# Kernel tuning notes

Hardware: AMD Instinct MI355X
Metric: run time of the kernel (lower is better)

The kernel has to match this reference:

```python
import jax, jax.numpy as jnp
from jax import lax
import numpy as np

B, F_BINS, T_TOTAL = 32, 128, 2400
H = 256           # cell_size
SEG = 24          # segment_size
S = T_TOTAL // SEG  # num_segments (T divisible by SEG)
SCALE = 1.0 / np.sqrt(H)


def _lstm_params(key, in_dim, hid_dim):
    k1, k2, k3, k4 = jax.random.split(key, 4)
    return (jax.random.normal(k1, (4 * hid_dim, in_dim), jnp.float32) * SCALE,
            jax.random.normal(k2, (4 * hid_dim, hid_dim), jnp.float32) * SCALE,
            jax.random.normal(k3, (4 * hid_dim,), jnp.float32) * SCALE,
            jax.random.normal(k4, (4 * hid_dim,), jnp.float32) * SCALE)


def setup_inputs() -> dict:
    key = jax.random.key(0)
    ks = jax.random.split(key, 5)
    inp = jax.random.normal(ks[0], (B, F_BINS, T_TOTAL), jnp.float32)
    oe = _lstm_params(ks[1], F_BINS, H)   # outer_encoder
    ie = _lstm_params(ks[2], H, H)        # inner_encoder
    idp = _lstm_params(ks[3], H, H)       # inner_decoder
    od = _lstm_params(ks[4], H, F_BINS)   # outer_decoder (hidden = input_size)
    d = {"inp": inp}
    for name, p in (("oe", oe), ("ie", ie), ("id", idp), ("od", od)):
        d[f"{name}_wih"], d[f"{name}_whh"], d[f"{name}_bih"], d[f"{name}_bhh"] = p
    return d


def run_lstm(x, w_ih, w_hh, b_ih, b_hh):
    """torch nn.LSTM (1 layer, batch_first). x: (N, T, I) -> outputs (N,T,Hd), h_T, c_T."""
    N = x.shape[0]
    Hd = w_hh.shape[1]
    # precompute input contribution for all steps: (N, T, 4H)
    xw = jnp.einsum('nti,gi->ntg', x, w_ih) + b_ih + b_hh

    def step(carry, xg):
        h, c = carry
        g = xg + h @ w_hh.T              # (N, 4H), gate order i,f,g,o
        i, f, gg, o = jnp.split(g, 4, axis=-1)
        c = jax.nn.sigmoid(f) * c + jax.nn.sigmoid(i) * jnp.tanh(gg)
        h = jax.nn.sigmoid(o) * jnp.tanh(c)
        return (h, c), h

    h0 = jnp.zeros((N, Hd), x.dtype)
    (hT, cT), ys = lax.scan(step, (h0, h0), jnp.swapaxes(xw, 0, 1))
    return jnp.swapaxes(ys, 0, 1), hT, cT


def reference(inp, oe_wih, oe_whh, oe_bih, oe_bhh,
              ie_wih, ie_whh, ie_bih, ie_bhh,
              id_wih, id_whh, id_bih, id_bhh,
              od_wih, od_whh, od_bih, od_bhh):
    x = jnp.swapaxes(inp, 1, 2)                      # (B, T, F)
    # outer encoder: all segments batched (independent in the original loop)
    segs = x.reshape(B * S, SEG, F_BINS)
    _, _, c_seg = run_lstm(segs, oe_wih, oe_whh, oe_bih, oe_bhh)   # (B*S, H)
    cell_state_tensor = c_seg.reshape(B, S, H)
    # inner encoder over segment cell-states -> bottleneck cell
    _, _, bottleneck = run_lstm(cell_state_tensor, ie_wih, ie_whh, ie_bih, ie_bhh)  # (B, H)
    # inner decoder: bottleneck repeated num_segments times
    dec_in = jnp.broadcast_to(bottleneck[:, None, :], (B, S, H))
    dec_out, _, _ = run_lstm(dec_in, id_wih, id_whh, id_bih, id_bhh)  # (B, S, H)
    # outer decoder: each segment code repeated SEG steps, batched over segments
    od_in = jnp.broadcast_to(dec_out.reshape(B * S, 1, H), (B * S, SEG, H))
    rec, _, _ = run_lstm(od_in, od_wih, od_whh, od_bih, od_bhh)       # (B*S, SEG, F)
    rec = rec.reshape(B, T_TOTAL, F_BINS)
    return jnp.swapaxes(rec, 1, 2)                   # (B, F, T)
```

## Files before the change

kernel.cpp:

```cpp
#include <hip/hip_runtime.h>


#define B_    32
#define F_    128
#define T_    2400
#define H_    256
#define SEG_  24
#define S_    100
#define NSEQ_ 3200

using v2h = __attribute__((ext_vector_type(2))) _Float16;
using v4h = __attribute__((ext_vector_type(4))) _Float16;
using v8h = __attribute__((ext_vector_type(8))) _Float16;
using v4f = __attribute__((ext_vector_type(4))) float;

#ifndef __has_builtin
#define __has_builtin(x) 0
#endif

__device__ __forceinline__ float fdot2f(v2h a, v2h b, float c) {
#if __has_builtin(__builtin_amdgcn_fdot2)
  return __builtin_amdgcn_fdot2(a, b, c, false);
#else
  return c + (float)a[0] * (float)b[0] + (float)a[1] * (float)b[1];
#endif
}

__device__ __forceinline__ v2h ext8(v8h v, int e) {
  v2h r; r[0] = v[2 * e]; r[1] = v[2 * e + 1]; return r;
}
__device__ __forceinline__ v2h ext4(v4h v, int e) {
  v2h r; r[0] = v[2 * e]; r[1] = v[2 * e + 1]; return r;
}

__device__ __forceinline__ float sigm(float x) { return 1.f / (1.f + __expf(-x)); }
__device__ __forceinline__ float tanh_f(float x) { return 1.f - 2.f / (__expf(2.f * x) + 1.f); }

__global__ void k_wt2(v2h* __restrict__ dst, const float* __restrict__ w1, int K1,
                      const float* __restrict__ w2, int K2src, int G, int n) {
  int idx = blockIdx.x * 256 + threadIdx.x;
  if (idx >= n) return;
  int k2 = idx / G, g = idx - k2 * G;
  int k = 2 * k2;
  float v0, v1;
  if (k < K1) {
    v0 = w1[(size_t)g * K1 + k];
    v1 = w1[(size_t)g * K1 + k + 1];
  } else {
    int kk = k - K1;
    v0 = w2[(size_t)g * K2src + kk];
    v1 = w2[(size_t)g * K2src + kk + 1];
  }
  v2h r;
  r[0] = (_Float16)v0;
  r[1] = (_Float16)v1;
  dst[idx] = r;
}

__global__ void k_f16(_Float16* __restrict__ dst, const float* __restrict__ src, int n) {
  int i = blockIdx.x * 256 + threadIdx.x;
  if (i < n) dst[i] = (_Float16)src[i];
}

__global__ void k_wpack_oe(v8h* __restrict__ dst, const float* __restrict__ wih,
                           const float* __restrict__ whh) {
  int idx = blockIdx.x * 256 + threadIdx.x;
  if (idx >= 12 * 64 * 64) return;
  int lane = idx & 63;
  int nt = (idx >> 6) & 63;
  int kc = idx >> 12;
  int col = nt * 16 + (lane & 15);
  int k0 = kc * 32 + (lane >> 4) * 8;
  v8h r;
#pragma unroll
  for (int j = 0; j < 8; ++j) {
    int k = k0 + j;
    float v = (k < 128) ? wih[(size_t)col * 128 + k] : whh[(size_t)col * 256 + (k - 128)];
    r[j] = (_Float16)v;
  }
  dst[idx] = r;
}

__global__ void k_wpack_od(v8h* __restrict__ dst, const float* __restrict__ whh) {
  int idx = blockIdx.x * 256 + threadIdx.x;
  if (idx >= 4 * 32 * 64) return;
  int lane = idx & 63;
  int nt = (idx >> 6) & 31;
  int kc = idx >> 11;
  int col = nt * 16 + (lane & 15);
  int k0 = kc * 32 + (lane >> 4) * 8;
  v8h r;
#pragma unroll
  for (int j = 0; j < 8; ++j) r[j] = (_Float16)whh[(size_t)col * 128 + k0 + j];
  dst[idx] = r;
}

__global__ void k_tin(const float* __restrict__ inp, _Float16* __restrict__ xT) {
  __shared__ float tile[32][33];
  int b = blockIdx.z, f0 = blockIdx.y * 32, t0 = blockIdx.x * 32;
  int tx = threadIdx.x, ty = threadIdx.y;
#pragma unroll
  for (int r = 0; r < 4; ++r) {
    int f = f0 + ty + 8 * r;
    tile[ty + 8 * r][tx] = inp[((size_t)b * F_ + f) * T_ + t0 + tx];
  }
  __syncthreads();
#pragma unroll
  for (int r = 0; r < 4; ++r) {
    int tau = t0 + ty + 8 * r;
    xT[((size_t)b * T_ + tau) * F_ + f0 + tx] = (_Float16)tile[tx][ty + 8 * r];
  }
}

__global__ void k_tout(const float* __restrict__ rec, float* __restrict__ out) {
  __shared__ float tile[32][33];
  int b = blockIdx.z, f0 = blockIdx.y * 32, t0 = blockIdx.x * 32;
  int tx = threadIdx.x, ty = threadIdx.y;
#pragma unroll
  for (int r = 0; r < 4; ++r) {
    int tau = t0 + ty + 8 * r;
    tile[ty + 8 * r][tx] = rec[((size_t)b * T_ + tau) * F_ + f0 + tx];
  }
  __syncthreads();
#pragma unroll
  for (int r = 0; r < 4; ++r) {
    int f = f0 + ty + 8 * r;
    out[((size_t)b * F_ + f) * T_ + t0 + tx] = tile[tx][ty + 8 * r];
  }
}

__global__ __launch_bounds__(512, 2) void k_outer_enc_mfma(
    const v8h* __restrict__ wpack,
    const _Float16* __restrict__ xT,
    const float* __restrict__ bih, const float* __restrict__ bhh,
    float* __restrict__ cst) {
  __shared__ __align__(16) _Float16 a2[32][392];
  const int tid = threadIdx.x;
  const int w = tid >> 6;
  const int lane = tid & 63;
  const int cI = lane & 15;
  const int q = lane >> 4;
  const int seq0 = blockIdx.x * 32;

  float bias[4][2];
#pragma unroll
  for (int g = 0; g < 4; ++g)
#pragma unroll
    for (int jt = 0; jt < 2; ++jt) {
      int col = g * 256 + w * 32 + jt * 16 + cI;
      bias[g][jt] = bih[col] + bhh[col];
    }

  for (int i = tid; i < 32 * 256; i += 512) a2[i >> 8][128 + (i & 255)] = (_Float16)0.f;
  {
    int row = tid >> 4, ch = tid & 15;
    v8h xv = ((const v8h*)(xT + ((size_t)(seq0 + row) * SEG_ + 0) * F_))[ch];
    *(v8h*)(&a2[row][ch * 8]) = xv;
  }
  __syncthreads();

  float cs[2][2][4];
#pragma unroll
  for (int mt = 0; mt < 2; ++mt)
#pragma unroll
    for (int jt = 0; jt < 2; ++jt)
#pragma unroll
      for (int r = 0; r < 4; ++r) cs[mt][jt][r] = 0.f;

  for (int t = 0; t < SEG_; ++t) {
    v4f C[2][8];
#pragma unroll
    for (int mt = 0; mt < 2; ++mt)
#pragma unroll
      for (int n = 0; n < 8; ++n) {
        v4f z = {0.f, 0.f, 0.f, 0.f};
        C[mt][n] = z;
      }
    v8h Bf[2][8];
#pragma unroll
    for (int n = 0; n < 8; ++n) {
      int nt = (n >> 1) * 16 + w * 2 + (n & 1);
      Bf[0][n] = wpack[(size_t)(0 * 64 + nt) * 64 + lane];
    }
#pragma unroll 2
    for (int kc = 0; kc < 12; ++kc) {
      int cur = kc & 1, nxt = cur ^ 1;
      if (kc < 11) {
#pragma unroll
        for (int n = 0; n < 8; ++n) {
          int nt = (n >> 1) * 16 + w * 2 + (n & 1);
          Bf[nxt][n] = wpack[(size_t)((kc + 1) * 64 + nt) * 64 + lane];
        }
      }
      v8h A0 = *(const v8h*)(&a2[0 * 16 + cI][kc * 32 + q * 8]);
      v8h A1 = *(const v8h*)(&a2[1 * 16 + cI][kc * 32 + q * 8]);
#pragma unroll
      for (int n = 0; n < 8; ++n) {
        C[0][n] = __builtin_amdgcn_mfma_f32_16x16x32_f16(A0, Bf[cur][n], C[0][n], 0, 0, 0);
        C[1][n] = __builtin_amdgcn_mfma_f32_16x16x32_f16(A1, Bf[cur][n], C[1][n], 0, 0, 0);
      }
    }
    __syncthreads();
#pragma unroll
    for (int mt = 0; mt < 2; ++mt)
#pragma unroll
      for (int jt = 0; jt < 2; ++jt)
#pragma unroll
        for (int r = 0; r < 4; ++r) {
          float gi = sigm(C[mt][0 * 2 + jt][r] + bias[0][jt]);
          float gf = sigm(C[mt][1 * 2 + jt][r] + bias[1][jt]);
          float gg = tanh_f(C[mt][2 * 2 + jt][r] + bias[2][jt]);
          float go = sigm(C[mt][3 * 2 + jt][r] + bias[3][jt]);
          float cc = gf * cs[mt][jt][r] + gi * gg;
          cs[mt][jt][r] = cc;
          float h = go * tanh_f(cc);
          a2[mt * 16 + q * 4 + r][128 + w * 32 + jt * 16 + cI] = (_Float16)h;
        }
    if (t < SEG_ - 1) {
      int row = tid >> 4, ch = tid & 15;
      v8h xv = ((const v8h*)(xT + ((size_t)(seq0 + row) * SEG_ + (t + 1)) * F_))[ch];
      *(v8h*)(&a2[row][ch * 8]) = xv;
    }
    __syncthreads();
  }
#pragma unroll
  for (int mt = 0; mt < 2; ++mt)
#pragma unroll
    for (int jt = 0; jt < 2; ++jt)
#pragma unroll
      for (int r = 0; r < 4; ++r)
        cst[(size_t)(seq0 + mt * 16 + q * 4 + r) * H_ + w * 32 + jt * 16 + cI] = cs[mt][jt][r];
}

__global__ __launch_bounds__(512, 2) void k_outer_dec_mfma(
    const v8h* __restrict__ wpack,
    const float* __restrict__ xw,
    float* __restrict__ rec) {
  __shared__ __align__(16) _Float16 ah[32][136];
  const int tid = threadIdx.x;
  const int w = tid >> 6;
  const int lane = tid & 63;
  const int cI = lane & 15;
  const int q = lane >> 4;
  const int seq0 = blockIdx.x * 32;

  v8h Bf[4][4];
#pragma unroll
  for (int kc = 0; kc < 4; ++kc)
#pragma unroll
    for (int g = 0; g < 4; ++g)
      Bf[kc][g] = wpack[(size_t)(kc * 32 + g * 8 + w) * 64 + lane];

  float xwr[2][4][4];
#pragma unroll
  for (int mt = 0; mt < 2; ++mt)
#pragma unroll
    for (int r = 0; r < 4; ++r) {
      int row = seq0 + mt * 16 + q * 4 + r;
#pragma unroll
      for (int g = 0; g < 4; ++g)
        xwr[mt][r][g] = xw[(size_t)row * 512 + g * 128 + w * 16 + cI];
    }

  for (int i = tid; i < 32 * 128; i += 512) ah[i >> 7][i & 127] = (_Float16)0.f;
  __syncthreads();

  float cs[2][4];
#pragma unroll
  for (int mt = 0; mt < 2; ++mt)
#pragma unroll
    for (int r = 0; r < 4; ++r) cs[mt][r] = 0.f;

  for (int t = 0; t < SEG_; ++t) {
    v4f C[2][4];
#pragma unroll
    for (int mt = 0; mt < 2; ++mt)
#pragma unroll
      for (int g = 0; g < 4; ++g) {
        v4f z = {0.f, 0.f, 0.f, 0.f};
        C[mt][g] = z;
      }
#pragma unroll
    for (int kc = 0; kc < 4; ++kc) {
      v8h A0 = *(const v8h*)(&ah[0 * 16 + cI][kc * 32 + q * 8]);
      v8h A1 = *(const v8h*)(&ah[1 * 16 + cI][kc * 32 + q * 8]);
#pragma unroll
      for (int g = 0; g < 4; ++g) {
        C[0][g] = __builtin_amdgcn_mfma_f32_16x16x32_f16(A0, Bf[kc][g], C[0][g], 0, 0, 0);
        C[1][g] = __builtin_amdgcn_mfma_f32_16x16x32_f16(A1, Bf[kc][g], C[1][g], 0, 0, 0);
      }
    }
    __syncthreads();
#pragma unroll
    for (int mt = 0; mt < 2; ++mt)
#pragma unroll
      for (int r = 0; r < 4; ++r) {
        float gi = sigm(C[mt][0][r] + xwr[mt][r][0]);
        float gf = sigm(C[mt][1][r] + xwr[mt][r][1]);
        float gg = tanh_f(C[mt][2][r] + xwr[mt][r][2]);
        float go = sigm(C[mt][3][r] + xwr[mt][r][3]);
        float cc = gf * cs[mt][r] + gi * gg;
        cs[mt][r] = cc;
        float h = go * tanh_f(cc);
        int row = mt * 16 + q * 4 + r;
        ah[row][w * 16 + cI] = (_Float16)h;
        rec[((size_t)(seq0 + row) * SEG_ + t) * 128 + w * 16 + cI] = h;
      }
    __syncthreads();
  }
}

template <int GT>
__global__ __launch_bounds__(256) void k_proj(
    const float* __restrict__ A, const v2h* __restrict__ wt2,
    const float* __restrict__ b1, const float* __restrict__ b2,
    float* __restrict__ out) {
  constexpr int G = GT * 256;
  __shared__ __align__(16) _Float16 a2[16][256];
  const int tid = threadIdx.x;
  const size_t row0 = (size_t)blockIdx.x * 16;
  for (int idx = tid; idx < 16 * 256; idx += 256) {
    int r = idx >> 8, k = idx & 255;
    a2[r][k] = (_Float16)A[(row0 + (size_t)r) * 256 + k];
  }
  __syncthreads();
  float acc[16][GT];
#pragma unroll
  for (int r = 0; r < 16; ++r)
#pragma unroll
    for (int q = 0; q < GT; ++q) acc[r][q] = 0.f;
  const v2h* wp = wt2 + tid;
#pragma unroll 2
  for (int k2 = 0; k2 < 128; ++k2) {
    v2h w[GT];
#pragma unroll
    for (int q = 0; q < GT; ++q) w[q] = wp[256 * q];
    wp += G;
#pragma unroll
    for (int r = 0; r < 16; ++r) {
      v2h a = ((const v2h*)&a2[r][0])[k2];
#pragma unroll
      for (int q = 0; q < GT; ++q) acc[r][q] = fdot2f(w[q], a, acc[r][q]);
    }
  }
#pragma unroll
  for (int q = 0; q < GT; ++q) {
    float bias = b1[tid + 256 * q] + b2[tid + 256 * q];
#pragma unroll
    for (int r = 0; r < 16; ++r)
      out[(row0 + (size_t)r) * G + tid + 256 * q] = acc[r][q] + bias;
  }
}

__global__ __launch_bounds__(512) void k_inner(
    const _Float16* __restrict__ whh,
    const float* __restrict__ xw, long xw_seq_stride, long xw_t_stride, int T,
    float* __restrict__ h_out,
    float* __restrict__ c_out) {
  __shared__ __align__(16) _Float16 ah[H_];
  __shared__ __align__(16) _Float16 wo[H_][260];
  const int t_ = threadIdx.x;
  const int p = t_ >> 1;
  const int hf = t_ & 1;
  const int b = blockIdx.x;

  v8h wv[3][16];
#pragma unroll
  for (int r = 0; r < 3; ++r) {
    const v8h* src = (const v8h*)(whh + ((size_t)(H_ * r + p)) * H_ + hf * 128);
#pragma unroll
    for (int q = 0; q < 16; ++q) wv[r][q] = src[q];
  }
  {
    const v4h* src = (const v4h*)(whh + ((size_t)(H_ * 3 + p)) * H_ + hf * 128);
    v4h* dst = (v4h*)&wo[p][hf * 128];
#pragma unroll
    for (int q = 0; q < 32; ++q) dst[q] = src[q];
  }
  if (t_ < H_) ah[t_] = (_Float16)0.f;
  float c = 0.f;
  __syncthreads();

  for (int t = 0; t < T; ++t) {
    const float* xwp = xw + (size_t)b * xw_seq_stride + (size_t)t * xw_t_stride;
    float x0 = xwp[p], x1 = xwp[H_ + p], x2 = xwp[2 * H_ + p], x3 = xwp[3 * H_ + p];
    float a0 = 0.f, a1 = 0.f, a2 = 0.f, a3 = 0.f;
    const v8h* A8 = ((const v8h*)ah) + hf * 16;
    const v4h* O4 = (const v4h*)&wo[p][hf * 128];
#pragma unroll
    for (int q = 0; q < 16; ++q) {
      v8h av = A8[q];
      v8h w0v = wv[0][q], w1v = wv[1][q], w2v = wv[2][q];
      v4h o0 = O4[2 * q], o1 = O4[2 * q + 1];
#pragma unroll
      for (int e = 0; e < 4; ++e) {
        v2h ap = ext8(av, e);
        a0 = fdot2f(ext8(w0v, e), ap, a0);
        a1 = fdot2f(ext8(w1v, e), ap, a1);
        a2 = fdot2f(ext8(w2v, e), ap, a2);
        v2h op = (e < 2) ? ext4(o0, e) : ext4(o1, e - 2);
        a3 = fdot2f(op, ap, a3);
      }
    }
    a0 += __shfl_xor(a0, 1);
    a1 += __shfl_xor(a1, 1);
    a2 += __shfl_xor(a2, 1);
    a3 += __shfl_xor(a3, 1);
    float gi = sigm(a0 + x0);
    float gf = sigm(a1 + x1);
    float gg = tanh_f(a2 + x2);
    float go = sigm(a3 + x3);
    c = gf * c + gi * gg;
    float h = go * tanh_f(c);
    __syncthreads();
    if (hf == 0) {
      ah[p] = (_Float16)h;
      if (h_out) h_out[((size_t)b * T + t) * H_ + p] = h;
    }
    __syncthreads();
  }
  if (c_out && hf == 0) c_out[(size_t)b * H_ + p] = c;
}

extern "C" void kernel_launch(void* const* d_in, const int* in_sizes, int n_in,
                              void* d_out, int out_size, void* d_ws, size_t ws_size,
                              hipStream_t stream) {
  const float* inp    = (const float*)d_in[0];
  const float* oe_wih = (const float*)d_in[1];
  const float* oe_whh = (const float*)d_in[2];
  const float* oe_bih = (const float*)d_in[3];
  const float* oe_bhh = (const float*)d_in[4];
  const float* ie_wih = (const float*)d_in[5];
  const float* ie_whh = (const float*)d_in[6];
  const float* ie_bih = (const float*)d_in[7];
  const float* ie_bhh = (const float*)d_in[8];
  const float* id_wih = (const float*)d_in[9];
  const float* id_whh = (const float*)d_in[10];
  const float* id_bih = (const float*)d_in[11];
  const float* id_bhh = (const float*)d_in[12];
  const float* od_wih = (const float*)d_in[13];
  const float* od_whh = (const float*)d_in[14];
  const float* od_bih = (const float*)d_in[15];
  const float* od_bhh = (const float*)d_in[16];

  char* ws = (char*)d_ws;
  _Float16* xT     = (_Float16*)(ws + 0);
  v8h* wpack_oe    = (v8h*)(ws + 19660800);
  float* cst       = (float*)(ws + 20447232);
  v2h* wt2_ie      = (v2h*)(ws + 23724032);
  float* xw_ie     = (float*)(ws + 24248320);
  _Float16* whh_ie = (_Float16*)(ws + 37355520);
  float* bott      = (float*)(ws + 37879808);
  v2h* wt2_id      = (v2h*)(ws + 37912576);
  float* xw_id     = (float*)(ws + 38436864);
  _Float16* whh_id = (_Float16*)(ws + 38567936);
  float* dec       = (float*)(ws + 39092224);
  v2h* wt2_odih    = (v2h*)(ws + 42369024);
  float* xw_od     = (float*)(ws + 42631168);
  v8h* wpack_od    = (v8h*)(ws + 49184768);
  float* rec       = (float*)(ws + 49315840);

  k_wpack_oe<<<dim3(192), dim3(256), 0, stream>>>(wpack_oe, oe_wih, oe_whh);
  k_wt2<<<dim3(512), dim3(256), 0, stream>>>(wt2_ie, ie_wih, 256, nullptr, 0, 1024, 128 * 1024);
  k_wt2<<<dim3(512), dim3(256), 0, stream>>>(wt2_id, id_wih, 256, nullptr, 0, 1024, 128 * 1024);
  k_wt2<<<dim3(256), dim3(256), 0, stream>>>(wt2_odih, od_wih, 256, nullptr, 0, 512, 128 * 512);
  k_wpack_od<<<dim3(32), dim3(256), 0, stream>>>(wpack_od, od_whh);
  k_f16<<<dim3(1024), dim3(256), 0, stream>>>(whh_ie, ie_whh, 262144);
  k_f16<<<dim3(1024), dim3(256), 0, stream>>>(whh_id, id_whh, 262144);

  k_tin<<<dim3(75, 4, 32), dim3(32, 8), 0, stream>>>(inp, xT);
  k_outer_enc_mfma<<<dim3(100), dim3(512), 0, stream>>>(wpack_oe, xT, oe_bih, oe_bhh, cst);
  k_proj<4><<<dim3(200), dim3(256), 0, stream>>>(cst, wt2_ie, ie_bih, ie_bhh, xw_ie);
  k_inner<<<dim3(32), dim3(512), 0, stream>>>(whh_ie, xw_ie, (long)S_ * 1024, 1024, S_, nullptr, bott);
  k_proj<4><<<dim3(2), dim3(256), 0, stream>>>(bott, wt2_id, id_bih, id_bhh, xw_id);
  k_inner<<<dim3(32), dim3(512), 0, stream>>>(whh_id, xw_id, 1024, 0, S_, dec, nullptr);
  k_proj<2><<<dim3(200), dim3(256), 0, stream>>>(dec, wt2_odih, od_bih, od_bhh, xw_od);
  k_outer_dec_mfma<<<dim3(100), dim3(512), 0, stream>>>(wpack_od, xw_od, rec);
  k_tout<<<dim3(75, 4, 32), dim3(32, 8), 0, stream>>>(rec, (float*)d_out);

  (void)in_sizes; (void)n_in; (void)out_size; (void)ws_size;
}
```

Baseline: 988.1 us.

## Use LDS-only barriers, deeper weight prefetch, early x loads, wider LDS reads

Replaces __syncthreads with an inline s_waitcnt lgkmcnt(0) plus s_barrier, so barriers no longer wait on outstanding global stores. The outer encoder now keeps a triple-buffered weight prefetch that is fully unrolled and carried across timesteps, and it issues the next timestep's input load before the MFMA loop. The inner kernel reads the o-gate weights from LDS as 8-wide vectors with padding 264, and it hoists the constant input projection out of the time loop when the time stride is zero. The risks are higher register pressure from the extra buffers and a barrier that relies on global stores not being consumed inside the kernel.

Measured after the change: 1.387 ms. 1.4x slower.

```diff
diff --git a/kernel.cpp b/kernel.cpp
--- a/kernel.cpp
+++ b/kernel.cpp
@@ -9,6 +9,8 @@
 #define S_    100
 #define NSEQ_ 3200
 
+#define BARRIER_LGKM() asm volatile("s_waitcnt lgkmcnt(0)\n\ts_barrier" ::: "memory")
+
 using v2h = __attribute__((ext_vector_type(2))) _Float16;
 using v4h = __attribute__((ext_vector_type(4))) _Float16;
 using v8h = __attribute__((ext_vector_type(8))) _Float16;
@@ -27,9 +29,6 @@
 }
 
 __device__ __forceinline__ v2h ext8(v8h v, int e) {
-  v2h r; r[0] = v[2 * e]; r[1] = v[2 * e + 1]; return r;
-}
-__device__ __forceinline__ v2h ext4(v4h v, int e) {
   v2h r; r[0] = v[2 * e]; r[1] = v[2 * e + 1]; return r;
 }
 
@@ -167,7 +166,20 @@
 #pragma unroll
       for (int r = 0; r < 4; ++r) cs[mt][jt][r] = 0.f;
 
+  const v8h* wp = wpack + lane;
+  v8h Bf[3][8];
+#pragma unroll
+  for (int n = 0; n < 8; ++n) {
+    int nt = (n >> 1) * 16 + w * 2 + (n & 1);
+    Bf[0][n] = wp[(size_t)(0 * 64 + nt) * 64];
+    Bf[1][n] = wp[(size_t)(1 * 64 + nt) * 64];
+  }
+
+  const int row = tid >> 4, ch = tid & 15;
   for (int t = 0; t < SEG_; ++t) {
+    int tn = (t + 1 < SEG_) ? t + 1 : t;
+    v8h xv = ((const v8h*)(xT + ((size_t)(seq0 + row) * SEG_ + tn) * F_))[ch];
+
     v4f C[2][8];
 #pragma unroll
     for (int mt = 0; mt < 2; ++mt)
@@ -176,31 +188,25 @@
         v4f z = {0.f, 0.f, 0.f, 0.f};
         C[mt][n] = z;
       }
-    v8h Bf[2][8];
-#pragma unroll
-    for (int n = 0; n < 8; ++n) {
-      int nt = (n >> 1) * 16 + w * 2 + (n & 1);
-      Bf[0][n] = wpack[(size_t)(0 * 64 + nt) * 64 + lane];
-    }
-#pragma unroll 2
+#pragma unroll
     for (int kc = 0; kc < 12; ++kc) {
-      int cur = kc & 1, nxt = cur ^ 1;
-      if (kc < 11) {
-#pragma unroll
-        for (int n = 0; n < 8; ++n) {
-          int nt = (n >> 1) * 16 + w * 2 + (n & 1);
-          Bf[nxt][n] = wpack[(size_t)((kc + 1) * 64 + nt) * 64 + lane];
-        }
+      const int pf = (kc + 2) % 12;
+      const int spf = (kc + 2) % 3;
+      const int scur = kc % 3;
+#pragma unroll
+      for (int n = 0; n < 8; ++n) {
+        int nt = (n >> 1) * 16 + w * 2 + (n & 1);
+        Bf[spf][n] = wp[(size_t)(pf * 64 + nt) * 64];
       }
       v8h A0 = *(const v8h*)(&a2[0 * 16 + cI][kc * 32 + q * 8]);
       v8h A1 = *(const v8h*)(&a2[1 * 16 + cI][kc * 32 + q * 8]);
 #pragma unroll
       for (int n = 0; n < 8; ++n) {
-        C[0][n] = __builtin_amdgcn_mfma_f32_16x16x32_f16(A0, Bf[cur][n], C[0][n], 0, 0, 0);
-        C[1][n] = __builtin_amdgcn_mfma_f32_16x16x32_f16(A1, Bf[cur][n], C[1][n], 0, 0, 0);
-      }
-    }
-    __syncthreads();
+        C[0][n] = __builtin_amdgcn_mfma_f32_16x16x32_f16(A0, Bf[scur][n], C[0][n], 0, 0, 0);
+        C[1][n] = __builtin_amdgcn_mfma_f32_16x16x32_f16(A1, Bf[scur][n], C[1][n], 0, 0, 0);
+      }
+    }
+    BARRIER_LGKM();
 #pragma unroll
     for (int mt = 0; mt < 2; ++mt)
 #pragma unroll
@@ -216,12 +222,8 @@
           float h = go * tanh_f(cc);
           a2[mt * 16 + q * 4 + r][128 + w * 32 + jt * 16 + cI] = (_Float16)h;
         }
-    if (t < SEG_ - 1) {
-      int row = tid >> 4, ch = tid & 15;
-      v8h xv = ((const v8h*)(xT + ((size_t)(seq0 + row) * SEG_ + (t + 1)) * F_))[ch];
-      *(v8h*)(&a2[row][ch * 8]) = xv;
-    }
-    __syncthreads();
+    if (t < SEG_ - 1) *(v8h*)(&a2[row][ch * 8]) = xv;
+    BARRIER_LGKM();
   }
 #pragma unroll
   for (int mt = 0; mt < 2; ++mt)
@@ -290,7 +292,7 @@
         C[1][g] = __builtin_amdgcn_mfma_f32_16x16x32_f16(A1, Bf[kc][g], C[1][g], 0, 0, 0);
       }
     }
-    __syncthreads();
+    BARRIER_LGKM();
 #pragma unroll
     for (int mt = 0; mt < 2; ++mt)
 #pragma unroll
@@ -306,7 +308,7 @@
         ah[row][w * 16 + cI] = (_Float16)h;
         rec[((size_t)(seq0 + row) * SEG_ + t) * 128 + w * 16 + cI] = h;
       }
-    __syncthreads();
+    BARRIER_LGKM();
   }
 }
 
@@ -358,7 +360,7 @@
     float* __restrict__ h_out,
     float* __restrict__ c_out) {
   __shared__ __align__(16) _Float16 ah[H_];
-  __shared__ __align__(16) _Float16 wo[H_][260];
+  __shared__ __align__(16) _Float16 wo[H_][264];
   const int t_ = threadIdx.x;
   const int p = t_ >> 1;
   const int hf = t_ & 1;
@@ -372,34 +374,42 @@
     for (int q = 0; q < 16; ++q) wv[r][q] = src[q];
   }
   {
-    const v4h* src = (const v4h*)(whh + ((size_t)(H_ * 3 + p)) * H_ + hf * 128);
-    v4h* dst = (v4h*)&wo[p][hf * 128];
-#pragma unroll
-    for (int q = 0; q < 32; ++q) dst[q] = src[q];
+    const v8h* src = (const v8h*)(whh + ((size_t)(H_ * 3 + p)) * H_ + hf * 128);
+    v8h* dst = (v8h*)&wo[p][hf * 128];
+#pragma unroll
+    for (int q = 0; q < 16; ++q) dst[q] = src[q];
   }
   if (t_ < H_) ah[t_] = (_Float16)0.f;
   float c = 0.f;
   __syncthreads();
 
+  const bool cx = (xw_t_stride == 0);
+  float x0 = 0.f, x1 = 0.f, x2 = 0.f, x3 = 0.f;
+  if (cx) {
+    const float* xwp = xw + (size_t)b * xw_seq_stride;
+    x0 = xwp[p]; x1 = xwp[H_ + p]; x2 = xwp[2 * H_ + p]; x3 = xwp[3 * H_ + p];
+  }
+
   for (int t = 0; t < T; ++t) {
-    const float* xwp = xw + (size_t)b * xw_seq_stride + (size_t)t * xw_t_stride;
-    float x0 = xwp[p], x1 = xwp[H_ + p], x2 = xwp[2 * H_ + p], x3 = xwp[3 * H_ + p];
+    if (!cx) {
+      const float* xwp = xw + (size_t)b * xw_seq_stride + (size_t)t * xw_t_stride;
+      x0 = xwp[p]; x1 = xwp[H_ + p]; x2 = xwp[2 * H_ + p]; x3 = xwp[3 * H_ + p];
+    }
     float a0 = 0.f, a1 = 0.f, a2 = 0.f, a3 = 0.f;
     const v8h* A8 = ((const v8h*)ah) + hf * 16;
-    const v4h* O4 = (const v4h*)&wo[p][hf * 128];
+    const v8h* O8 = (const v8h*)&wo[p][hf * 128];
 #pragma unroll
     for (int q = 0; q < 16; ++q) {
       v8h av = A8[q];
+      v8h ov = O8[q];
       v8h w0v = wv[0][q], w1v = wv[1][q], w2v = wv[2][q];
-      v4h o0 = O4[2 * q], o1 = O4[2 * q + 1];
 #pragma unroll
       for (int e = 0; e < 4; ++e) {
         v2h ap = ext8(av, e);
         a0 = fdot2f(ext8(w0v, e), ap, a0);
         a1 = fdot2f(ext8(w1v, e), ap, a1);
         a2 = fdot2f(ext8(w2v, e), ap, a2);
-        v2h op = (e < 2) ? ext4(o0, e) : ext4(o1, e - 2);
-        a3 = fdot2f(op, ap, a3);
+        a3 = fdot2f(ext8(ov, e), ap, a3);
       }
     }
     a0 += __shfl_xor(a0, 1);
@@ -412,12 +422,12 @@
     float go = sigm(a3 + x3);
     c = gf * c + gi * gg;
     float h = go * tanh_f(c);
-    __syncthreads();
+    BARRIER_LGKM();
     if (hf == 0) {
       ah[p] = (_Float16)h;
       if (h_out) h_out[((size_t)b * T + t) * H_ + p] = h;
     }
-    __syncthreads();
+    BARRIER_LGKM();
   }
   if (c_out && hf == 0) c_out[(size_t)b * H_ + p] = c;
 }
```
